# Performance work log

Hardware: AMD Instinct MI355X
Metric: run time of the kernel (lower is better)

The kernel has to match this reference:

```python
import jax, jax.numpy as jnp
import numpy as np

DEPTH = 4  # init kwarg 'depth'
H = 256   # init kwarg 'hidden_size'
ATOM_FDIM, BOND_FDIM = 35, 5


def _build_graph(rng, N, E):
    src = rng.integers(0, N, E).astype(np.int32)
    dst = rng.integers(0, N, E).astype(np.int32)
    # line graph (backtracking=False): lg edge e1 -> e2 iff dst[e1]==src[e2] and src[e1]!=dst[e2]
    indeg = np.bincount(dst, minlength=N)
    idx_sorted = np.argsort(dst, kind='stable')          # edge ids grouped by dst node
    ptr = np.concatenate([[0], np.cumsum(indeg)]).astype(np.int64)
    counts = indeg[src]                                   # in-edges of src[e] feed edge e
    total = int(counts.sum())
    lg_dst = np.repeat(np.arange(E, dtype=np.int64), counts)
    cum = np.cumsum(counts) - counts
    within = np.arange(total) - np.repeat(cum, counts)
    lg_src = idx_sorted[np.repeat(ptr[src], counts) + within]
    keep = src[lg_src] != dst[lg_dst]                     # drop backtracking pairs
    return src, dst, lg_src[keep].astype(np.int32), lg_dst[keep].astype(np.int32)


def setup_inputs() -> dict:
    rng = np.random.default_rng(0)
    N, E, Et, K, G = 50000, 200000, 100000, 50000, 2000
    src, dst, lg_src, lg_dst = _build_graph(rng, N, E)
    graph_ids = ((np.arange(N, dtype=np.int64) * G) // N).astype(np.int32)
    f32 = lambda *s: rng.standard_normal(s).astype(np.float32)
    return {
        'x_nodes': jnp.asarray(f32(N, ATOM_FDIM)),
        'x_edges': jnp.asarray(rng.random((E, BOND_FDIM)).astype(np.float32)),
        'tree_m': jnp.asarray(f32(Et, H) * 0.1),
        'W_i': jnp.asarray(f32(ATOM_FDIM + BOND_FDIM, H) * 0.05),
        'W_h': jnp.asarray(f32(H, H) * 0.05),
        'W_o': jnp.asarray(f32(ATOM_FDIM + H, H) * 0.05),
        'b_o': jnp.asarray(f32(H) * 0.05),
        'edge_src': jnp.asarray(src),
        'edge_dst': jnp.asarray(dst),
        'lg_src': jnp.asarray(lg_src),
        'lg_dst': jnp.asarray(lg_dst),
        'tgt_nodes': jnp.asarray(rng.integers(0, N, K).astype(np.int32)),
        'tree_eid': jnp.asarray(rng.integers(0, Et, K).astype(np.int32)),
        'graph_ids': jnp.asarray(graph_ids),
        'n_graphs': G,
    }


def reference(x_nodes, x_edges, tree_m, W_i, W_h, W_o, b_o,
              edge_src, edge_dst, lg_src, lg_dst, tgt_nodes, tree_eid,
              graph_ids, n_graphs):
    N = x_nodes.shape[0]
    E = x_edges.shape[0]
    # edge input features: [src atom feats | bond feats] @ W_i (no bias)
    msg_input = jnp.concatenate([x_nodes[edge_src], x_edges], axis=1) @ W_i  # [E,H]
    msg = jax.nn.relu(msg_input)
    # tree message alignment: scatter-add tree edge messages onto cand nodes
    node_alpha = jnp.zeros((N, msg.shape[1]), msg.dtype).at[tgt_nodes].add(tree_m[tree_eid])
    edge_alpha = node_alpha[edge_src]  # apply_edges: alpha = src alpha
    # loopy BP over the line graph
    for _ in range(DEPTH - 1):
        accum = jax.ops.segment_sum(msg[lg_src], lg_dst, num_segments=E)  # [E,H]
        msg = jax.nn.relu(msg_input + (accum + edge_alpha) @ W_h)
    # gather: m = sum of incoming edge messages per node
    m = jax.ops.segment_sum(msg, edge_dst, num_segments=N)  # [N,H]
    h = jax.nn.relu(jnp.concatenate([x_nodes, m + node_alpha], axis=1) @ W_o + b_o)
    # mean_nodes per candidate graph
    sums = jax.ops.segment_sum(h, graph_ids, num_segments=n_graphs)
    cnt = jax.ops.segment_sum(jnp.ones((N, 1), h.dtype), graph_ids, num_segments=n_graphs)
    return sums / jnp.maximum(cnt, 1.0)
```

## Files before the change

### kernel.cpp

```cpp
#include <hip/hip_runtime.h>
#include <stdint.h>

typedef unsigned short u16;
typedef __attribute__((ext_vector_type(8))) short bf16x8;
typedef __attribute__((ext_vector_type(4))) float f32x4;

#define HD 256
#define AST 264
#define CORR_CAP 2048

static __device__ __forceinline__ float b2f(u16 x){
  union{float f; unsigned u;} v; v.u = ((unsigned)x)<<16; return v.f;
}
static __device__ __forceinline__ u16 f2b(float f){
  union{float f; unsigned u;} v; v.f = f;
  unsigned r = v.u + 0x7fffu + ((v.u>>16)&1u);
  return (u16)(r>>16);
}
static __device__ __forceinline__ void acc4(float* a, uint2 v){
  a[0] += b2f((u16)v.x); a[1] += b2f((u16)(v.x>>16));
  a[2] += b2f((u16)v.y); a[3] += b2f((u16)(v.y>>16));
}

__global__ void k_zero_int(int* __restrict__ p, int n){
  int i = blockIdx.x*256 + threadIdx.x;
  if (i < n) p[i] = 0;
}

__global__ void k_hist(const int* __restrict__ key, int* __restrict__ deg, int n){
  int i = blockIdx.x*256 + threadIdx.x;
  if (i < n) atomicAdd(&deg[key[i]], 1);
}

__global__ void k_scan_p1(const int* __restrict__ deg, int n, int* __restrict__ bsum){
  int i = blockIdx.x*256 + threadIdx.x;
  int v = (i < n) ? deg[i] : 0;
  #pragma unroll
  for (int o=32; o>0; o>>=1) v += __shfl_down(v, o);
  __shared__ int w[4];
  if ((threadIdx.x&63)==0) w[threadIdx.x>>6] = v;
  __syncthreads();
  if (threadIdx.x==0) bsum[blockIdx.x] = w[0]+w[1]+w[2]+w[3];
}
__global__ __launch_bounds__(1024) void k_scan_p2(int* __restrict__ bsum, int nb,
                                                  int* __restrict__ total_dst){
  __shared__ int sm[1024];
  int t = threadIdx.x;
  int v = (t < nb) ? bsum[t] : 0;
  sm[t] = v; __syncthreads();
  for (int o=1; o<1024; o<<=1){
    int u = (t>=o) ? sm[t-o] : 0;
    __syncthreads();
    sm[t] += u;
    __syncthreads();
  }
  if (t < nb) bsum[t] = sm[t] - v;
  if (t == 1023 && total_dst) *total_dst = sm[1023];
}
__global__ void k_scan_p3(const int* __restrict__ deg, const int* __restrict__ bsum, int n,
                          int* __restrict__ start, int* __restrict__ cursor){
  int t = threadIdx.x;
  int i = blockIdx.x*256 + t;
  int v = (i < n) ? deg[i] : 0;
  __shared__ int sm[256];
  sm[t] = v; __syncthreads();
  for (int o=1; o<256; o<<=1){
    int u = (t>=o) ? sm[t-o] : 0;
    __syncthreads();
    sm[t] += u;
    __syncthreads();
  }
  int ex = sm[t] - v + bsum[blockIdx.x];
  if (i < n){ start[i] = ex; cursor[i] = ex; }
}

__global__ void k_fill(const int* __restrict__ key, const int* __restrict__ val,
                       int* __restrict__ cursor, int* __restrict__ bucket, int n){
  int i = blockIdx.x*256 + threadIdx.x;
  if (i >= n) return;
  int pos = atomicAdd(&cursor[key[i]], 1);
  bucket[pos] = val ? val[i] : i;
}

__global__ void k_permarr(const int* __restrict__ perm, const int* __restrict__ esrc,
                          const int* __restrict__ edst, int* __restrict__ esrc_p,
                          int* __restrict__ edst_p, int E){
  int e = blockIdx.x*256 + threadIdx.x;
  if (e >= E) return;
  int o = perm[e];
  esrc_p[e] = esrc[o];
  edst_p[e] = edst[o];
}

__global__ void k_xep(const float* __restrict__ xe, const int* __restrict__ perm,
                      float* __restrict__ xep, int E){
  int e = blockIdx.x*256 + threadIdx.x;
  if (e >= E) return;
  int o = perm[e];
  #pragma unroll
  for (int k=0;k<5;k++) xep[(size_t)e*5+k] = xe[(size_t)o*5+k];
}

__global__ void k_xnf(const float* __restrict__ xn, u16* __restrict__ xnf, int N){
  int g = blockIdx.x*256 + threadIdx.x;
  int v2 = g >> 6, c = g & 63;
  if (v2 >= N) return;
  float v = (c < 35) ? xn[(size_t)v2*35 + c] : 0.f;
  xnf[g] = f2b(v);
}

__global__ void k_alpha_gather(const float* __restrict__ tree_m, const int* __restrict__ start,
                               const int* __restrict__ bucket, u16* __restrict__ alpha16, int N){
  int v = (int)(((long long)blockIdx.x*blockDim.x + threadIdx.x)>>6);
  int l = threadIdx.x & 63;
  if (v >= N) return;
  int s = start[v], e2 = start[v+1];
  float a0=0.f,a1=0.f,a2=0.f,a3=0.f;
  for (int j=s;j<e2;j++){
    float4 tv = *(const float4*)(tree_m + (size_t)bucket[j]*HD + l*4);
    a0 += tv.x; a1 += tv.y; a2 += tv.z; a3 += tv.w;
  }
  ushort4 o; o.x=f2b(a0); o.y=f2b(a1); o.z=f2b(a2); o.w=f2b(a3);
  *(ushort4*)(alpha16 + (size_t)v*HD + l*4) = o;
}

__global__ void k_prep_frag(const float* __restrict__ W, int k0, int kmax, int nks,
                            u16* __restrict__ out){
  int g = blockIdx.x*256 + threadIdx.x;
  if (g >= nks*16*512) return;
  int i = g & 7, l = (g>>3)&63, t = g>>9;
  int nj = t & 15, ks = t >> 4;
  int n = nj*16 + (l&15);
  int k = ks*32 + (l>>4)*8 + i;
  float v = (k < kmax) ? W[(size_t)(k0+k)*HD + n] : 0.f;
  out[g] = f2b(v);
}

__global__ __launch_bounds__(512, 4) void k_pr_gemm(
    const u16* __restrict__ featA, const u16* __restrict__ BTf,
    u16* __restrict__ out16, int M)
{
  const int tid = threadIdx.x;
  const int w = tid>>6, l = tid&63;
  const int lr = l&15, lq = l>>4;
  const int nrb = (M+15)>>4;
  bf16x8 B0[2], B1[2];
  #pragma unroll
  for (int ks=0; ks<2; ks++){
    B0[ks] = *(const bf16x8*)(BTf + (size_t)((ks*16 + w*2  )*512) + l*8);
    B1[ks] = *(const bf16x8*)(BTf + (size_t)((ks*16 + w*2+1)*512) + l*8);
  }
  const int c0 = w*32 + lr, c1 = w*32 + 16 + lr;
  for (int rb = blockIdx.x; rb < nrb; rb += gridDim.x){
    int r = rb*16 + lr; int rc = min(r, M-1);
    const u16* fr = featA + (size_t)rc*64 + lq*8;
    bf16x8 a0 = *(const bf16x8*)(fr);
    bf16x8 a1 = *(const bf16x8*)(fr + 32);
    f32x4 acc0 = (f32x4){0.f,0.f,0.f,0.f};
    f32x4 acc1 = (f32x4){0.f,0.f,0.f,0.f};
    acc0 = __builtin_amdgcn_mfma_f32_16x16x32_bf16(a0, B0[0], acc0, 0,0,0);
    acc0 = __builtin_amdgcn_mfma_f32_16x16x32_bf16(a1, B0[1], acc0, 0,0,0);
    acc1 = __builtin_amdgcn_mfma_f32_16x16x32_bf16(a0, B1[0], acc1, 0,0,0);
    acc1 = __builtin_amdgcn_mfma_f32_16x16x32_bf16(a1, B1[1], acc1, 0,0,0);
    #pragma unroll
    for (int reg=0; reg<4; reg++){
      int gm = rb*16 + lq*4 + reg;
      if (gm < M){
        out16[(size_t)gm*HD + c0] = f2b(acc0[reg]);
        out16[(size_t)gm*HD + c1] = f2b(acc1[reg]);
      }
    }
  }
}

__global__ __launch_bounds__(512, 4) void k_nodeU(
    const u16* __restrict__ msg, const u16* __restrict__ alpha16,
    const int* __restrict__ start_d, const u16* __restrict__ BTf,
    const u16* __restrict__ Padd, const float* __restrict__ bias,
    u16* __restrict__ out16, float* __restrict__ out32, int N, int mode)
{
  __shared__ u16 A_lds[16][AST];
  const int tid = threadIdx.x;
  const int w = tid>>6, l = tid&63;
  const int lr = l&15, lq = l>>4;
  const int ngrp = (N+15)>>4;

  bf16x8 B0[8], B1[8];
  #pragma unroll
  for (int ks=0; ks<8; ks++){
    B0[ks] = *(const bf16x8*)(BTf + (size_t)((ks*16 + w*2  )*512) + l*8);
    B1[ks] = *(const bf16x8*)(BTf + (size_t)((ks*16 + w*2+1)*512) + l*8);
  }
  const int c0 = w*32 + lr, c1 = w*32 + 16 + lr;
  float b0 = 0.f, b1 = 0.f;
  if (mode == 1){ b0 = bias[c0]; b1 = bias[c1]; }

  for (int grp = blockIdx.x; grp < ngrp; grp += gridDim.x){
    const int vb = grp*16;
    #pragma unroll
    for (int h=0; h<2; h++){
      int v = vb + w*2 + h;
      float a[4] = {0.f,0.f,0.f,0.f};
      if (v < N){
        uint2 av = *(const uint2*)(alpha16 + (size_t)v*HD + l*4);
        a[0]=b2f((u16)av.x); a[1]=b2f((u16)(av.x>>16));
        a[2]=b2f((u16)av.y); a[3]=b2f((u16)(av.y>>16));
        int s = start_d[v], e2 = start_d[v+1];
        const u16* ml = msg + (size_t)s*HD + l*4;
        int cnt = e2 - s, j = 0;
        for (; j+2 <= cnt; j+=2){
          uint2 v0 = *(const uint2*)(ml);
          uint2 v1 = *(const uint2*)(ml + HD);
          ml += 2*HD;
          acc4(a, v0); acc4(a, v1);
        }
        for (; j < cnt; j++){
          uint2 v0 = *(const uint2*)(ml); ml += HD;
          acc4(a, v0);
        }
      }
      ushort4 o; o.x=f2b(a[0]); o.y=f2b(a[1]); o.z=f2b(a[2]); o.w=f2b(a[3]);
      *(ushort4*)&A_lds[w*2+h][l*4] = o;
    }
    __syncthreads();
    f32x4 acc0 = (f32x4){0.f,0.f,0.f,0.f};
    f32x4 acc1 = (f32x4){0.f,0.f,0.f,0.f};
    const u16* Ar = &A_lds[lr][0];
    #pragma unroll
    for (int ks=0; ks<8; ks++){
      bf16x8 af = *(const bf16x8*)(Ar + ks*32 + lq*8);
      acc0 = __builtin_amdgcn_mfma_f32_16x16x32_bf16(af, B0[ks], acc0, 0,0,0);
      acc1 = __builtin_amdgcn_mfma_f32_16x16x32_bf16(af, B1[ks], acc1, 0,0,0);
    }
    #pragma unroll
    for (int reg=0; reg<4; reg++){
      int gm = vb + lq*4 + reg;
      if (gm < N){
        float v0 = acc0[reg] + b2f(Padd[(size_t)gm*HD + c0]);
        float v1 = acc1[reg] + b2f(Padd[(size_t)gm*HD + c1]);
        if (mode == 1){
          v0 += b0; v1 += b1;
          out32[(size_t)gm*HD + c0] = v0 > 0.f ? v0 : 0.f;
          out32[(size_t)gm*HD + c1] = v1 > 0.f ? v1 : 0.f;
        } else {
          out16[(size_t)gm*HD + c0] = f2b(v0);
          out16[(size_t)gm*HD + c1] = f2b(v1);
        }
      }
    }
    __syncthreads();
  }
}

__global__ __launch_bounds__(256, 8) void k_edge_update(
    const u16* __restrict__ U, const float* __restrict__ xep,
    const int* __restrict__ esrc_p, const float* __restrict__ Wi,
    u16* __restrict__ msg, int E)
{
  const int l = threadIdx.x & 63;
  const int wid = (blockIdx.x*256 + threadIdx.x) >> 6;
  const int nw = gridDim.x*4;
  float wq[5][4];
  #pragma unroll
  for (int k=0;k<5;k++){
    float4 t = *(const float4*)(Wi + (size_t)(35+k)*HD + l*4);
    wq[k][0]=t.x; wq[k][1]=t.y; wq[k][2]=t.z; wq[k][3]=t.w;
  }
  for (int e = wid; e < E; e += nw){
    int s = esrc_p[e];
    const float* xp = xep + (size_t)e*5;
    float x0=xp[0], x1=xp[1], x2=xp[2], x3=xp[3], x4=xp[4];
    uint2 uv = *(const uint2*)(U + (size_t)s*HD + l*4);
    float v[4] = { b2f((u16)uv.x), b2f((u16)(uv.x>>16)),
                   b2f((u16)uv.y), b2f((u16)(uv.y>>16)) };
    #pragma unroll
    for (int j=0;j<4;j++){
      float q = x0*wq[0][j] + x1*wq[1][j] + x2*wq[2][j] + x3*wq[3][j] + x4*wq[4][j];
      float r = v[j] + q;
      v[j] = r > 0.f ? r : 0.f;
    }
    ushort4 o; o.x=f2b(v[0]); o.y=f2b(v[1]); o.z=f2b(v[2]); o.w=f2b(v[3]);
    *(ushort4*)(msg + (size_t)e*HD + l*4) = o;
  }
}

__global__ void k_pairs(const int* __restrict__ esrc_p, const int* __restrict__ edst_p,
                        const int* __restrict__ start_d,
                        int* __restrict__ npairs, int2* __restrict__ pairs, int E){
  int e = blockIdx.x*256 + threadIdx.x;
  if (e >= E) return;
  int u = esrc_p[e], v = edst_p[e];
  int s = start_d[u], t = start_d[u+1];
  for (int ep=s; ep<t; ep++){
    if (esrc_p[ep] == v){
      int pos = atomicAdd(npairs, 1);
      if (pos < CORR_CAP) pairs[pos] = (int2){e, ep};
    }
  }
}

__global__ void k_snapshot(const u16* __restrict__ msg, const int2* __restrict__ pairs,
                           const int* __restrict__ npairs_p, u16* __restrict__ corrbuf){
  int np = *npairs_p; if (np > CORR_CAP) np = CORR_CAP;
  int wid = (blockIdx.x*256 + threadIdx.x) >> 6;
  int l = threadIdx.x & 63;
  int nw = gridDim.x * 4;
  for (int p = wid; p < np; p += nw){
    int ep = pairs[p].y;
    *(uint2*)(corrbuf + (size_t)p*HD + l*4) =
        *(const uint2*)(msg + (size_t)ep*HD + l*4);
  }
}

__global__ __launch_bounds__(256) void k_fixup(
    const u16* __restrict__ U, const float* __restrict__ xep,
    const int* __restrict__ esrc_p,
    const u16* __restrict__ corrbuf, const int2* __restrict__ pairs,
    const int* __restrict__ npairs_p, const float* __restrict__ Wi,
    const float* __restrict__ Wh, u16* __restrict__ msg){
  int np = *npairs_p; if (np > CORR_CAP) np = CORR_CAP;
  int t = threadIdx.x;
  __shared__ float cs[256];
  for (int p = blockIdx.x; p < np; p += gridDim.x){
    int e = pairs[p].x;
    bool first = true;
    for (int q=0;q<p;q++) if (pairs[q].x == e){ first = false; break; }
    if (!first) continue;
    float c = 0.f;
    for (int q=p;q<np;q++) if (pairs[q].x == e) c += b2f(corrbuf[(size_t)q*HD + t]);
    cs[t] = c; __syncthreads();
    float corr = 0.f;
    for (int k=0;k<HD;k++) corr += cs[k]*Wh[(size_t)k*HD + t];
    const float* xp = xep + (size_t)e*5;
    float qv = 0.f;
    for (int k=0;k<5;k++) qv += xp[k]*Wi[(size_t)(35+k)*HD + t];
    int u = esrc_p[e];
    float val = b2f(U[(size_t)u*HD + t]) + qv - corr;
    msg[(size_t)e*HD + t] = f2b(val > 0.f ? val : 0.f);
    __syncthreads();
  }
}

__global__ void k_graph_mean(const float* __restrict__ h, const int* __restrict__ gid,
                             int N, int G, float* __restrict__ out){
  int g = (int)(((long long)blockIdx.x*blockDim.x + threadIdx.x)>>6);
  int l = threadIdx.x & 63;
  if (g >= G) return;
  int lo=0, hi=N;
  while (lo<hi){ int mid=(lo+hi)>>1; if (gid[mid] < g) lo=mid+1; else hi=mid; }
  int b = lo;
  hi = N;
  while (lo<hi){ int mid=(lo+hi)>>1; if (gid[mid] < g+1) lo=mid+1; else hi=mid; }
  int e2 = lo;
  float a0=0.f,a1=0.f,a2=0.f,a3=0.f;
  for (int v=b; v<e2; v++){
    float4 hv = *(const float4*)(h + (size_t)v*HD + l*4);
    a0 += hv.x; a1 += hv.y; a2 += hv.z; a3 += hv.w;
  }
  int cnt = e2 - b; if (cnt < 1) cnt = 1;
  float inv = 1.0f/(float)cnt;
  float4 o; o.x=a0*inv; o.y=a1*inv; o.z=a2*inv; o.w=a3*inv;
  *(float4*)(out + (size_t)g*HD + l*4) = o;
}

extern "C" void kernel_launch(void* const* d_in, const int* in_sizes, int n_in,
                              void* d_out, int out_size, void* d_ws, size_t ws_size,
                              hipStream_t stream){
  const float* x_nodes = (const float*)d_in[0];
  const float* x_edges = (const float*)d_in[1];
  const float* tree_m  = (const float*)d_in[2];
  const float* W_i     = (const float*)d_in[3];
  const float* W_h     = (const float*)d_in[4];
  const float* W_o     = (const float*)d_in[5];
  const float* b_o     = (const float*)d_in[6];
  const int* edge_src = (const int*)d_in[7];
  const int* edge_dst = (const int*)d_in[8];
  const int* tgt      = (const int*)d_in[11];
  const int* teid     = (const int*)d_in[12];
  const int* gid      = (const int*)d_in[13];

  const int N = in_sizes[0]/35;
  const int E = in_sizes[1]/5;
  const int K = in_sizes[11];
  const int G = out_size/HD;

  char* wsb = (char*)d_ws;
  auto align256 = [](size_t x){ return (x + 255) & ~(size_t)255; };
  size_t oMsg    = 0;
  size_t oAlpha  = oMsg    + align256((size_t)E*HD*2);
  size_t oU      = oAlpha  + align256((size_t)N*HD*2);
  size_t oP      = oU      + align256((size_t)N*HD*2);
  size_t oR      = oP      + align256((size_t)N*HD*2);
  size_t oXnf    = oR      + align256((size_t)N*HD*2);
  size_t oXep    = oXnf    + align256((size_t)N*64*2);
  size_t oBTP    = oXep    + align256((size_t)E*5*4);
  size_t oBTWh   = oBTP    + align256((size_t)2*16*512*2);
  size_t oBTRa   = oBTWh   + align256((size_t)8*16*512*2);
  size_t oBTWob  = oBTRa   + align256((size_t)2*16*512*2);
  size_t oDegD   = oBTWob  + align256((size_t)8*16*512*2);
  size_t oStartD = oDegD   + align256((size_t)(N+1)*4);
  size_t oCurD   = oStartD + align256((size_t)(N+1)*4);
  size_t oPerm   = oCurD   + align256((size_t)N*4);
  size_t oEsrcP  = oPerm   + align256((size_t)E*4);
  size_t oEdstP  = oEsrcP  + align256((size_t)E*4);
  size_t oDegT   = oEdstP  + align256((size_t)E*4);
  size_t oStartT = oDegT   + align256((size_t)N*4);
  size_t oCurT   = oStartT + align256((size_t)(N+1)*4);
  size_t oBukT   = oCurT   + align256((size_t)N*4);
  size_t oBsum   = oBukT   + align256((size_t)K*4);
  size_t oPairs  = oBsum   + align256((size_t)1024*4);
  size_t oCorrB  = oPairs  + align256((size_t)CORR_CAP*8);

  u16*   msg     = (u16*)(wsb + oMsg);
  u16*   alpha16 = (u16*)(wsb + oAlpha);
  u16*   U       = (u16*)(wsb + oU);
  u16*   P       = (u16*)(wsb + oP);
  u16*   R       = (u16*)(wsb + oR);
  u16*   xnf     = (u16*)(wsb + oXnf);
  float* xep     = (float*)(wsb + oXep);
  u16*   BT_P    = (u16*)(wsb + oBTP);
  u16*   BT_Wh   = (u16*)(wsb + oBTWh);
  u16*   BT_Ra   = (u16*)(wsb + oBTRa);
  u16*   BT_Wob  = (u16*)(wsb + oBTWob);
  int*   deg_d   = (int*)(wsb + oDegD);
  int*   npairs  = deg_d + N;
  int*   start_d = (int*)(wsb + oStartD);
  int*   cur_d   = (int*)(wsb + oCurD);
  int*   perm    = (int*)(wsb + oPerm);
  int*   esrc_p  = (int*)(wsb + oEsrcP);
  int*   edst_p  = (int*)(wsb + oEdstP);
  int*   deg_t   = (int*)(wsb + oDegT);
  int*   start_t = (int*)(wsb + oStartT);
  int*   cur_t   = (int*)(wsb + oCurT);
  int*   buk_t   = (int*)(wsb + oBukT);
  int*   bsum    = (int*)(wsb + oBsum);
  int2*  pairs   = (int2*)(wsb + oPairs);
  u16*   corrbuf = (u16*)(wsb + oCorrB);
  float* hbuf    = (float*)(wsb + oU);

  const int egrid256 = (E+255)/256;
  const int kgrid256 = (K+255)/256;
  const int ngrid256 = (N+255)/256;
  const int nbN      = (N+255)/256;

  k_prep_frag<<<64,  256, 0, stream>>>(W_i, 0, 35, 2, BT_P);
  k_prep_frag<<<256, 256, 0, stream>>>(W_h, 0, 256, 8, BT_Wh);
  k_prep_frag<<<64,  256, 0, stream>>>(W_o, 0, 35, 2, BT_Ra);
  k_prep_frag<<<256, 256, 0, stream>>>(W_o, 35, 256, 8, BT_Wob);

  k_zero_int<<<(N+1+255)/256, 256, 0, stream>>>(deg_d, N+1);
  k_hist<<<egrid256, 256, 0, stream>>>(edge_dst, deg_d, E);
  k_scan_p1<<<nbN, 256, 0, stream>>>(deg_d, N, bsum);
  k_scan_p2<<<1, 1024, 0, stream>>>(bsum, nbN, start_d + N);
  k_scan_p3<<<nbN, 256, 0, stream>>>(deg_d, bsum, N, start_d, cur_d);
  k_fill<<<egrid256, 256, 0, stream>>>(edge_dst, (const int*)0, cur_d, perm, E);
  k_permarr<<<egrid256, 256, 0, stream>>>(perm, edge_src, edge_dst, esrc_p, edst_p, E);
  k_xep<<<egrid256, 256, 0, stream>>>(x_edges, perm, xep, E);
  k_xnf<<<((size_t)N*64+255)/256, 256, 0, stream>>>(x_nodes, xnf, N);

  k_zero_int<<<ngrid256, 256, 0, stream>>>(deg_t, N);
  k_hist<<<kgrid256, 256, 0, stream>>>(tgt, deg_t, K);
  k_scan_p1<<<nbN, 256, 0, stream>>>(deg_t, N, bsum);
  k_scan_p2<<<1, 1024, 0, stream>>>(bsum, nbN, start_t + N);
  k_scan_p3<<<nbN, 256, 0, stream>>>(deg_t, bsum, N, start_t, cur_t);
  k_fill<<<kgrid256, 256, 0, stream>>>(tgt, teid, cur_t, buk_t, K);
  k_alpha_gather<<<(N+3)/4, 256, 0, stream>>>(tree_m, start_t, buk_t, alpha16, N);

  k_pairs<<<egrid256, 256, 0, stream>>>(esrc_p, edst_p, start_d, npairs, pairs, E);

  k_pr_gemm<<<512, 512, 0, stream>>>(xnf, BT_P, P, N);
  k_pr_gemm<<<512, 512, 0, stream>>>(xnf, BT_Ra, R, N);

  k_edge_update<<<2048, 256, 0, stream>>>(P, xep, esrc_p, W_i, msg, E);

  for (int it=0; it<3; ++it){
    k_nodeU<<<512, 512, 0, stream>>>(msg, alpha16, start_d, BT_Wh, P,
                                     (const float*)0, U, (float*)0, N, 0);
    k_snapshot<<<32, 256, 0, stream>>>(msg, pairs, npairs, corrbuf);
    k_edge_update<<<2048, 256, 0, stream>>>(U, xep, esrc_p, W_i, msg, E);
    k_fixup<<<64, 256, 0, stream>>>(U, xep, esrc_p, corrbuf, pairs, npairs,
                                    W_i, W_h, msg);
  }

  k_nodeU<<<512, 512, 0, stream>>>(msg, alpha16, start_d, BT_Wob, R,
                                   b_o, (u16*)0, hbuf, N, 1);
  k_graph_mean<<<(G+3)/4, 256, 0, stream>>>(hbuf, gid, N, G, (float*)d_out);
}
```

Baseline: 640.0 us.

## Reformulate loopy BP in node space to avoid materializing per-edge messages

```diff
diff --git a/kernel.cpp b/kernel.cpp
--- a/kernel.cpp
+++ b/kernel.cpp
@@ -17,9 +17,19 @@
   unsigned r = v.u + 0x7fffu + ((v.u>>16)&1u);
   return (u16)(r>>16);
 }
-static __device__ __forceinline__ void acc4(float* a, uint2 v){
-  a[0] += b2f((u16)v.x); a[1] += b2f((u16)(v.x>>16));
-  a[2] += b2f((u16)v.y); a[3] += b2f((u16)(v.y>>16));
+static __device__ __forceinline__ void racc2(float* a, uint2 iv, uint2 vv){
+  float t0 = b2f((u16)iv.x)       + b2f((u16)vv.x);
+  float t1 = b2f((u16)(iv.x>>16)) + b2f((u16)(vv.x>>16));
+  float t2 = b2f((u16)iv.y)       + b2f((u16)vv.y);
+  float t3 = b2f((u16)(iv.y>>16)) + b2f((u16)(vv.y>>16));
+  a[0] += t0>0.f?t0:0.f; a[1] += t1>0.f?t1:0.f;
+  a[2] += t2>0.f?t2:0.f; a[3] += t3>0.f?t3:0.f;
+}
+static __device__ __forceinline__ void racc1(float* a, uint2 iv){
+  float t0 = b2f((u16)iv.x), t1 = b2f((u16)(iv.x>>16));
+  float t2 = b2f((u16)iv.y), t3 = b2f((u16)(iv.y>>16));
+  a[0] += t0>0.f?t0:0.f; a[1] += t1>0.f?t1:0.f;
+  a[2] += t2>0.f?t2:0.f; a[3] += t3>0.f?t3:0.f;
 }
 
 __global__ void k_zero_int(int* __restrict__ p, int n){
@@ -173,11 +183,68 @@
   }
 }
 
-__global__ __launch_bounds__(512, 4) void k_nodeU(
-    const u16* __restrict__ msg, const u16* __restrict__ alpha16,
-    const int* __restrict__ start_d, const u16* __restrict__ BTf,
-    const u16* __restrict__ Padd, const float* __restrict__ bias,
-    u16* __restrict__ out16, float* __restrict__ out32, int N, int mode)
+__global__ __launch_bounds__(256, 8) void k_build_I(
+    const u16* __restrict__ P, const float* __restrict__ xep,
+    const int* __restrict__ esrc_p, const float* __restrict__ Wi,
+    u16* __restrict__ I, int E)
+{
+  const int l = threadIdx.x & 63;
+  const int wid = (blockIdx.x*256 + threadIdx.x) >> 6;
+  const int nw = gridDim.x*4;
+  float wq[5][4];
+  #pragma unroll
+  for (int k=0;k<5;k++){
+    float4 t = *(const float4*)(Wi + (size_t)(35+k)*HD + l*4);
+    wq[k][0]=t.x; wq[k][1]=t.y; wq[k][2]=t.z; wq[k][3]=t.w;
+  }
+  for (int e = wid; e < E; e += nw){
+    int s = esrc_p[e];
+    const float* xp = xep + (size_t)e*5;
+    float x0=xp[0], x1=xp[1], x2=xp[2], x3=xp[3], x4=xp[4];
+    uint2 uv = *(const uint2*)(P + (size_t)s*HD + l*4);
+    float v[4] = { b2f((u16)uv.x), b2f((u16)(uv.x>>16)),
+                   b2f((u16)uv.y), b2f((u16)(uv.y>>16)) };
+    #pragma unroll
+    for (int j=0;j<4;j++)
+      v[j] += x0*wq[0][j] + x1*wq[1][j] + x2*wq[2][j] + x3*wq[3][j] + x4*wq[4][j];
+    ushort4 o; o.x=f2b(v[0]); o.y=f2b(v[1]); o.z=f2b(v[2]); o.w=f2b(v[3]);
+    *(ushort4*)(I + (size_t)e*HD + l*4) = o;
+  }
+}
+
+__global__ void k_pairs(const int* __restrict__ esrc_p, const int* __restrict__ edst_p,
+                        const int* __restrict__ start_d,
+                        int* __restrict__ npairs, int2* __restrict__ pairs, int E){
+  int e = blockIdx.x*256 + threadIdx.x;
+  if (e >= E) return;
+  int u = esrc_p[e], v = edst_p[e];
+  int s = start_d[u], t = start_d[u+1];
+  for (int ep=s; ep<t; ep++){
+    if (esrc_p[ep] == v){
+      int pos = atomicAdd(npairs, 1);
+      if (pos < CORR_CAP) pairs[pos] = (int2){e, ep};
+    }
+  }
+}
+
+__global__ void k_msgA0(const u16* __restrict__ I, const int2* __restrict__ pairs,
+                        const int* __restrict__ npairs_p, float* __restrict__ msgA){
+  int np = *npairs_p; if (np > CORR_CAP) np = CORR_CAP;
+  int t = threadIdx.x;
+  for (int p = blockIdx.x; p < np; p += gridDim.x){
+    int ep = pairs[p].y;
+    float v = b2f(I[(size_t)ep*HD + t]);
+    msgA[(size_t)p*HD + t] = v > 0.f ? v : 0.f;
+  }
+}
+
+__global__ __launch_bounds__(512, 4) void k_bp(
+    const u16* __restrict__ I, const u16* __restrict__ Vprev,
+    const u16* __restrict__ alpha16, const int* __restrict__ start_d,
+    const int* __restrict__ esrc_p, const u16* __restrict__ BTf,
+    const u16* __restrict__ Radd, const float* __restrict__ bias,
+    u16* __restrict__ Sout, u16* __restrict__ Vout, float* __restrict__ hout,
+    int N, int mode)
 {
   __shared__ u16 A_lds[16][AST];
   const int tid = threadIdx.x;
@@ -198,29 +265,48 @@
   for (int grp = blockIdx.x; grp < ngrp; grp += gridDim.x){
     const int vb = grp*16;
     #pragma unroll
-    for (int h=0; h<2; h++){
-      int v = vb + w*2 + h;
+    for (int hh=0; hh<2; hh++){
+      int v = vb + w*2 + hh;
       float a[4] = {0.f,0.f,0.f,0.f};
       if (v < N){
         uint2 av = *(const uint2*)(alpha16 + (size_t)v*HD + l*4);
         a[0]=b2f((u16)av.x); a[1]=b2f((u16)(av.x>>16));
         a[2]=b2f((u16)av.y); a[3]=b2f((u16)(av.y>>16));
         int s = start_d[v], e2 = start_d[v+1];
-        const u16* ml = msg + (size_t)s*HD + l*4;
-        int cnt = e2 - s, j = 0;
-        for (; j+2 <= cnt; j+=2){
-          uint2 v0 = *(const uint2*)(ml);
-          uint2 v1 = *(const uint2*)(ml + HD);
-          ml += 2*HD;
-          acc4(a, v0); acc4(a, v1);
-        }
-        for (; j < cnt; j++){
-          uint2 v0 = *(const uint2*)(ml); ml += HD;
-          acc4(a, v0);
+        int cnt = e2 - s;
+        const u16* Ir = I + (size_t)s*HD + l*4;
+        if (Vprev){
+          const int* sp = esrc_p + s;
+          int j = 0;
+          for (; j+2 <= cnt; j+=2){
+            int s0 = sp[j], s1 = sp[j+1];
+            uint2 i0 = *(const uint2*)(Ir);
+            uint2 i1 = *(const uint2*)(Ir + HD);
+            uint2 v0 = *(const uint2*)(Vprev + (size_t)s0*HD + l*4);
+            uint2 v1 = *(const uint2*)(Vprev + (size_t)s1*HD + l*4);
+            Ir += 2*HD;
+            racc2(a, i0, v0); racc2(a, i1, v1);
+          }
+          if (j < cnt){
+            int s0 = sp[j];
+            uint2 i0 = *(const uint2*)(Ir);
+            uint2 v0 = *(const uint2*)(Vprev + (size_t)s0*HD + l*4);
+            racc2(a, i0, v0);
+          }
+        } else {
+          int j = 0;
+          for (; j+2 <= cnt; j+=2){
+            uint2 i0 = *(const uint2*)(Ir);
+            uint2 i1 = *(const uint2*)(Ir + HD);
+            Ir += 2*HD;
+            racc1(a, i0); racc1(a, i1);
+          }
+          if (j < cnt) racc1(a, *(const uint2*)(Ir));
         }
       }
       ushort4 o; o.x=f2b(a[0]); o.y=f2b(a[1]); o.z=f2b(a[2]); o.w=f2b(a[3]);
-      *(ushort4*)&A_lds[w*2+h][l*4] = o;
+      if (v < N) *(ushort4*)(Sout + (size_t)v*HD + l*4) = o;
+      *(ushort4*)&A_lds[w*2+hh][l*4] = o;
     }
     __syncthreads();
     f32x4 acc0 = (f32x4){0.f,0.f,0.f,0.f};
@@ -236,15 +322,14 @@
     for (int reg=0; reg<4; reg++){
       int gm = vb + lq*4 + reg;
       if (gm < N){
-        float v0 = acc0[reg] + b2f(Padd[(size_t)gm*HD + c0]);
-        float v1 = acc1[reg] + b2f(Padd[(size_t)gm*HD + c1]);
         if (mode == 1){
-          v0 += b0; v1 += b1;
-          out32[(size_t)gm*HD + c0] = v0 > 0.f ? v0 : 0.f;
-          out32[(size_t)gm*HD + c1] = v1 > 0.f ? v1 : 0.f;
+          float v0 = acc0[reg] + b2f(Radd[(size_t)gm*HD + c0]) + b0;
+          float v1 = acc1[reg] + b2f(Radd[(size_t)gm*HD + c1]) + b1;
+          hout[(size_t)gm*HD + c0] = v0 > 0.f ? v0 : 0.f;
+          hout[(size_t)gm*HD + c1] = v1 > 0.f ? v1 : 0.f;
         } else {
-          out16[(size_t)gm*HD + c0] = f2b(v0);
-          out16[(size_t)gm*HD + c1] = f2b(v1);
+          Vout[(size_t)gm*HD + c0] = f2b(acc0[reg]);
+          Vout[(size_t)gm*HD + c1] = f2b(acc1[reg]);
         }
       }
     }
@@ -252,91 +337,61 @@
   }
 }
 
-__global__ __launch_bounds__(256, 8) void k_edge_update(
-    const u16* __restrict__ U, const float* __restrict__ xep,
-    const int* __restrict__ esrc_p, const float* __restrict__ Wi,
-    u16* __restrict__ msg, int E)
+__global__ __launch_bounds__(256, 1) void k_correct(
+    const u16* __restrict__ I, const u16* __restrict__ Vprev,
+    const int* __restrict__ esrc_p, const int* __restrict__ edst_p,
+    const int2* __restrict__ pairs, const int* __restrict__ npairs_p,
+    const float* __restrict__ Wh, u16* __restrict__ Scur,
+    u16* __restrict__ Vcur, float* __restrict__ hout,
+    const float* __restrict__ Wob, const u16* __restrict__ Radd,
+    const float* __restrict__ bias,
+    float* __restrict__ msgA, float* __restrict__ newA, int isfinal)
 {
-  const int l = threadIdx.x & 63;
-  const int wid = (blockIdx.x*256 + threadIdx.x) >> 6;
-  const int nw = gridDim.x*4;
-  float wq[5][4];
-  #pragma unroll
-  for (int k=0;k<5;k++){
-    float4 t = *(const float4*)(Wi + (size_t)(35+k)*HD + l*4);
-    wq[k][0]=t.x; wq[k][1]=t.y; wq[k][2]=t.z; wq[k][3]=t.w;
-  }
-  for (int e = wid; e < E; e += nw){
-    int s = esrc_p[e];
-    const float* xp = xep + (size_t)e*5;
-    float x0=xp[0], x1=xp[1], x2=xp[2], x3=xp[3], x4=xp[4];
-    uint2 uv = *(const uint2*)(U + (size_t)s*HD + l*4);
-    float v[4] = { b2f((u16)uv.x), b2f((u16)(uv.x>>16)),
-                   b2f((u16)uv.y), b2f((u16)(uv.y>>16)) };
-    #pragma unroll
-    for (int j=0;j<4;j++){
-      float q = x0*wq[0][j] + x1*wq[1][j] + x2*wq[2][j] + x3*wq[3][j] + x4*wq[4][j];
-      float r = v[j] + q;
-      v[j] = r > 0.f ? r : 0.f;
-    }
-    ushort4 o; o.x=f2b(v[0]); o.y=f2b(v[1]); o.z=f2b(v[2]); o.w=f2b(v[3]);
-    *(ushort4*)(msg + (size_t)e*HD + l*4) = o;
-  }
-}
-
-__global__ void k_pairs(const int* __restrict__ esrc_p, const int* __restrict__ edst_p,
-                        const int* __restrict__ start_d,
-                        int* __restrict__ npairs, int2* __restrict__ pairs, int E){
-  int e = blockIdx.x*256 + threadIdx.x;
-  if (e >= E) return;
-  int u = esrc_p[e], v = edst_p[e];
-  int s = start_d[u], t = start_d[u+1];
-  for (int ep=s; ep<t; ep++){
-    if (esrc_p[ep] == v){
-      int pos = atomicAdd(npairs, 1);
-      if (pos < CORR_CAP) pairs[pos] = (int2){e, ep};
-    }
-  }
-}
-
-__global__ void k_snapshot(const u16* __restrict__ msg, const int2* __restrict__ pairs,
-                           const int* __restrict__ npairs_p, u16* __restrict__ corrbuf){
   int np = *npairs_p; if (np > CORR_CAP) np = CORR_CAP;
-  int wid = (blockIdx.x*256 + threadIdx.x) >> 6;
-  int l = threadIdx.x & 63;
-  int nw = gridDim.x * 4;
-  for (int p = wid; p < np; p += nw){
-    int ep = pairs[p].y;
-    *(uint2*)(corrbuf + (size_t)p*HD + l*4) =
-        *(const uint2*)(msg + (size_t)ep*HD + l*4);
-  }
-}
-
-__global__ __launch_bounds__(256) void k_fixup(
-    const u16* __restrict__ U, const float* __restrict__ xep,
-    const int* __restrict__ esrc_p,
-    const u16* __restrict__ corrbuf, const int2* __restrict__ pairs,
-    const int* __restrict__ npairs_p, const float* __restrict__ Wi,
-    const float* __restrict__ Wh, u16* __restrict__ msg){
-  int np = *npairs_p; if (np > CORR_CAP) np = CORR_CAP;
+  if (np == 0) return;
   int t = threadIdx.x;
-  __shared__ float cs[256];
-  for (int p = blockIdx.x; p < np; p += gridDim.x){
+  __shared__ float cs[HD];
+  __shared__ float sa[HD];
+  for (int p=0; p<np; p++){
     int e = pairs[p].x;
     bool first = true;
-    for (int q=0;q<p;q++) if (pairs[q].x == e){ first = false; break; }
+    for (int q=0;q<p;q++) if (pairs[q].x == e){ first=false; break; }
     if (!first) continue;
     float c = 0.f;
-    for (int q=p;q<np;q++) if (pairs[q].x == e) c += b2f(corrbuf[(size_t)q*HD + t]);
+    for (int q=p;q<np;q++) if (pairs[q].x == e) c += msgA[(size_t)q*HD + t];
     cs[t] = c; __syncthreads();
     float corr = 0.f;
     for (int k=0;k<HD;k++) corr += cs[k]*Wh[(size_t)k*HD + t];
-    const float* xp = xep + (size_t)e*5;
-    float qv = 0.f;
-    for (int k=0;k<5;k++) qv += xp[k]*Wi[(size_t)(35+k)*HD + t];
     int u = esrc_p[e];
-    float val = b2f(U[(size_t)u*HD + t]) + qv - corr;
-    msg[(size_t)e*HD + t] = f2b(val > 0.f ? val : 0.f);
+    float base = b2f(I[(size_t)e*HD + t]) + b2f(Vprev[(size_t)u*HD + t]);
+    float mn = base > 0.f ? base : 0.f;
+    float bt = base - corr;
+    float mt = bt > 0.f ? bt : 0.f;
+    int dv = edst_p[e];
+    u16* sp2 = Scur + (size_t)dv*HD + t;
+    *sp2 = f2b(b2f(*sp2) + mt - mn);
+    for (int q=0;q<np;q++) if (pairs[q].y == e) newA[(size_t)q*HD + t] = mt;
+    __syncthreads();
+  }
+  for (int p=0;p<np;p++) msgA[(size_t)p*HD + t] = newA[(size_t)p*HD + t];
+  __syncthreads();
+  for (int p=0; p<np; p++){
+    int dv = edst_p[pairs[p].x];
+    bool first = true;
+    for (int q=0;q<p;q++) if (edst_p[pairs[q].x] == dv){ first=false; break; }
+    if (!first) continue;
+    sa[t] = b2f(Scur[(size_t)dv*HD + t]);
+    __syncthreads();
+    if (!isfinal){
+      float acc2 = 0.f;
+      for (int k=0;k<HD;k++) acc2 += sa[k]*Wh[(size_t)k*HD + t];
+      Vcur[(size_t)dv*HD + t] = f2b(acc2);
+    } else {
+      float acc2 = 0.f;
+      for (int k=0;k<HD;k++) acc2 += sa[k]*Wob[(size_t)k*HD + t];
+      float hv = acc2 + b2f(Radd[(size_t)dv*HD + t]) + bias[t];
+      hout[(size_t)dv*HD + t] = hv > 0.f ? hv : 0.f;
+    }
     __syncthreads();
   }
 }
@@ -386,12 +441,14 @@
 
   char* wsb = (char*)d_ws;
   auto align256 = [](size_t x){ return (x + 255) & ~(size_t)255; };
-  size_t oMsg    = 0;
-  size_t oAlpha  = oMsg    + align256((size_t)E*HD*2);
-  size_t oU      = oAlpha  + align256((size_t)N*HD*2);
-  size_t oP      = oU      + align256((size_t)N*HD*2);
-  size_t oR      = oP      + align256((size_t)N*HD*2);
-  size_t oXnf    = oR      + align256((size_t)N*HD*2);
+  size_t oI      = 0;
+  size_t oSa     = oI      + align256((size_t)E*HD*2);
+  size_t oVa     = oSa     + align256((size_t)N*HD*2);
+  size_t oP      = oVa     + align256((size_t)N*HD*2);
+  size_t oVb     = oP      + align256((size_t)N*HD*2);
+  size_t oR      = oVb     + align256((size_t)N*HD*2);
+  size_t oAlpha  = oR      + align256((size_t)N*HD*2);
+  size_t oXnf    = oAlpha  + align256((size_t)N*HD*2);
   size_t oXep    = oXnf    + align256((size_t)N*64*2);
   size_t oBTP    = oXep    + align256((size_t)E*5*4);
   size_t oBTWh   = oBTP    + align256((size_t)2*16*512*2);
@@ -409,13 +466,16 @@
   size_t oBukT   = oCurT   + align256((size_t)N*4);
   size_t oBsum   = oBukT   + align256((size_t)K*4);
   size_t oPairs  = oBsum   + align256((size_t)1024*4);
-  size_t oCorrB  = oPairs  + align256((size_t)CORR_CAP*8);
-
-  u16*   msg     = (u16*)(wsb + oMsg);
+  size_t oMsgA   = oPairs  + align256((size_t)CORR_CAP*8);
+  size_t oNewA   = oMsgA   + align256((size_t)CORR_CAP*HD*4);
+
+  u16*   I       = (u16*)(wsb + oI);
+  u16*   Sa      = (u16*)(wsb + oSa);
+  u16*   Va      = (u16*)(wsb + oVa);
+  u16*   P       = (u16*)(wsb + oP);
+  u16*   Vb      = (u16*)(wsb + oVb);
+  u16*   R       = (u16*)(wsb + oR);
   u16*   alpha16 = (u16*)(wsb + oAlpha);
-  u16*   U       = (u16*)(wsb + oU);
-  u16*   P       = (u16*)(wsb + oP);
-  u16*   R       = (u16*)(wsb + oR);
   u16*   xnf     = (u16*)(wsb + oXnf);
   float* xep     = (float*)(wsb + oXep);
   u16*   BT_P    = (u16*)(wsb + oBTP);
@@ -435,8 +495,9 @@
   int*   buk_t   = (int*)(wsb + oBukT);
   int*   bsum    = (int*)(wsb + oBsum);
   int2*  pairs   = (int2*)(wsb + oPairs);
-  u16*   corrbuf = (u16*)(wsb + oCorrB);
-  float* hbuf    = (float*)(wsb + oU);
+  float* msgA    = (float*)(wsb + oMsgA);
+  float* newA    = (float*)(wsb + oNewA);
+  float* hbuf    = (float*)(wsb + oP);
 
   const int egrid256 = (E+255)/256;
   const int kgrid256 = (K+255)/256;
@@ -471,18 +532,27 @@
   k_pr_gemm<<<512, 512, 0, stream>>>(xnf, BT_P, P, N);
   k_pr_gemm<<<512, 512, 0, stream>>>(xnf, BT_Ra, R, N);
 
-  k_edge_update<<<2048, 256, 0, stream>>>(P, xep, esrc_p, W_i, msg, E);
-
-  for (int it=0; it<3; ++it){
-    k_nodeU<<<512, 512, 0, stream>>>(msg, alpha16, start_d, BT_Wh, P,
-                                     (const float*)0, U, (float*)0, N, 0);
-    k_snapshot<<<32, 256, 0, stream>>>(msg, pairs, npairs, corrbuf);
-    k_edge_update<<<2048, 256, 0, stream>>>(U, xep, esrc_p, W_i, msg, E);
-    k_fixup<<<64, 256, 0, stream>>>(U, xep, esrc_p, corrbuf, pairs, npairs,
-                                    W_i, W_h, msg);
-  }
-
-  k_nodeU<<<512, 512, 0, stream>>>(msg, alpha16, start_d, BT_Wob, R,
-                                   b_o, (u16*)0, hbuf, N, 1);
+  k_build_I<<<2048, 256, 0, stream>>>(P, xep, esrc_p, W_i, I, E);
+  k_msgA0<<<64, 256, 0, stream>>>(I, pairs, npairs, msgA);
+
+  const float* Wob = W_o + 35*HD;
+
+  k_bp<<<512, 512, 0, stream>>>(I, (const u16*)0, alpha16, start_d, esrc_p, BT_Wh,
+                                (const u16*)0, (const float*)0, Sa, Va, (float*)0, N, 0);
+  k_bp<<<512, 512, 0, stream>>>(I, Va, alpha16, start_d, esrc_p, BT_Wh,
+                                (const u16*)0, (const float*)0, Sa, Vb, (float*)0, N, 0);
+  k_correct<<<1, 256, 0, stream>>>(I, Va, esrc_p, edst_p, pairs, npairs, W_h, Sa,
+                                   Vb, (float*)0, (const float*)0, (const u16*)0,
+                                   (const float*)0, msgA, newA, 0);
+  k_bp<<<512, 512, 0, stream>>>(I, Vb, alpha16, start_d, esrc_p, BT_Wh,
+                                (const u16*)0, (const float*)0, Sa, Va, (float*)0, N, 0);
+  k_correct<<<1, 256, 0, stream>>>(I, Vb, esrc_p, edst_p, pairs, npairs, W_h, Sa,
+                                   Va, (float*)0, (const float*)0, (const u16*)0,
+                                   (const float*)0, msgA, newA, 0);
+  k_bp<<<512, 512, 0, stream>>>(I, Va, alpha16, start_d, esrc_p, BT_Wob,
+                                R, b_o, Sa, (u16*)0, hbuf, N, 1);
+  k_correct<<<1, 256, 0, stream>>>(I, Va, esrc_p, edst_p, pairs, npairs, W_h, Sa,
+                                   (u16*)0, hbuf, Wob, R, b_o, msgA, newA, 1);
+
   k_graph_mean<<<(G+3)/4, 256, 0, stream>>>(hbuf, gid, N, G, (float*)d_out);
 }
```

New measurement: 947.8 us. +48.1%, slower.
